# Kernel tuning notes

Hardware: AMD Instinct MI355X
Metric: run time of the kernel (lower is better)

## Reference

```python
import jax, jax.numpy as jnp
import numpy as np

N, F_IN, C, H, L = 4096, 768, 256, 4, 2
DH = C // H  # 64 per-head dim for GATv2


def _ln(x, g, b, eps=1e-5):
    mu = x.mean(-1, keepdims=True)
    var = ((x - mu) ** 2).mean(-1, keepdims=True)
    return (x - mu) / jnp.sqrt(var + eps) * g + b


def _gat_layer(x, wl, wr, att, b, src, dst):
    # GATv2Conv: e_ij = att . leaky_relu(Wl x_j + Wr x_i); softmax over incoming j; concat heads.
    xs = (x @ wl).reshape(N, H, DH)  # source transform
    xd = (x @ wr).reshape(N, H, DH)  # target transform
    e = jnp.einsum('ehd,hd->eh', jax.nn.leaky_relu(xs[src] + xd[dst], 0.2), att)  # [E,H]
    m = jax.ops.segment_max(e, dst, num_segments=N)          # segment softmax (stable)
    p = jnp.exp(e - m[dst])
    s = jax.ops.segment_sum(p, dst, num_segments=N)
    alpha = p / (s[dst] + 1e-16)                             # [E,H]
    out = jax.ops.segment_sum(alpha[:, :, None] * xs[src], dst, num_segments=N)
    return out.reshape(N, C) + b


def _mha(x, wq, wk, wv, bq, bk, bv, wo, bo):
    # nn.MultiheadAttention, batch=1 sequence of all news nodes, eval mode.
    q = (x @ wq + bq).reshape(N, H, DH)
    k = (x @ wk + bk).reshape(N, H, DH)
    v = (x @ wv + bv).reshape(N, H, DH)
    scale = np.float32(1.0 / np.sqrt(DH))
    a = jax.nn.softmax(jnp.einsum('nhd,mhd->hnm', q, k) * scale, axis=-1)  # [H,N,N]
    o = jnp.einsum('hnm,mhd->nhd', a, v).reshape(N, C)
    return o @ wo + bo


def setup_inputs() -> dict:
    key = jax.random.key(0)
    ks = jax.random.split(key, 32)
    rn = lambda k, shp: (jax.random.normal(k, shp, dtype=jnp.float32) * 0.02)
    inp = {
        'x': jax.random.normal(ks[0], (N, F_IN), dtype=jnp.float32),
        'edge_index': jax.random.randint(ks[1], (2, N * 64), 0, N, dtype=jnp.int64),
        'emb_w': rn(ks[2], (F_IN, C)), 'emb_b': jnp.zeros((C,), jnp.float32),
        'g1_wl': rn(ks[3], (C, C)), 'g1_wr': rn(ks[4], (C, C)),
        'g1_att': rn(ks[5], (H, DH)), 'g1_b': jnp.zeros((C,), jnp.float32),
        'g2_wl': rn(ks[6], (C, C)), 'g2_wr': rn(ks[7], (C, C)),
        'g2_att': rn(ks[8], (H, DH)), 'g2_b': jnp.zeros((C,), jnp.float32),
        'mha_wq': rn(ks[9], (C, C)), 'mha_wk': rn(ks[10], (C, C)), 'mha_wv': rn(ks[11], (C, C)),
        'mha_bq': jnp.zeros((C,), jnp.float32), 'mha_bk': jnp.zeros((C,), jnp.float32),
        'mha_bv': jnp.zeros((C,), jnp.float32),
        'mha_wo': rn(ks[12], (C, C)), 'mha_bo': jnp.zeros((C,), jnp.float32),
        'ln_g': jnp.ones((C,), jnp.float32), 'ln_b': jnp.zeros((C,), jnp.float32),
        'cls_w1': rn(ks[13], (C, C // 2)), 'cls_b1': jnp.zeros((C // 2,), jnp.float32),
        'cls_w2': rn(ks[14], (C // 2, 2)), 'cls_b2': jnp.zeros((2,), jnp.float32),
    }
    return inp


def reference(x, edge_index, emb_w, emb_b, g1_wl, g1_wr, g1_att, g1_b,
              g2_wl, g2_wr, g2_att, g2_b, mha_wq, mha_wk, mha_wv, mha_bq,
              mha_bk, mha_bv, mha_wo, mha_bo, ln_g, ln_b,
              cls_w1, cls_b1, cls_w2, cls_b2):
    # add self loops (GATv2Conv default add_self_loops=True)
    loops = jnp.arange(N, dtype=edge_index.dtype)
    src = jnp.concatenate([edge_index[0], loops])
    dst = jnp.concatenate([edge_index[1], loops])

    h = x @ emb_w + emb_b                              # node embedding Linear(-1, C)
    h = jax.nn.relu(_gat_layer(h, g1_wl, g1_wr, g1_att, g1_b, src, dst))
    h = jax.nn.relu(_gat_layer(h, g2_wl, g2_wr, g2_att, g2_b, src, dst))

    # entity-aware self-attention + residual LayerNorm
    enh = _mha(h, mha_wq, mha_wk, mha_wv, mha_bq, mha_bk, mha_bv, mha_wo, mha_bo)
    h = _ln(h + enh, ln_g, ln_b)

    # classifier MLP (dropout = identity in eval)
    h = jax.nn.relu(h @ cls_w1 + cls_b1)
    return h @ cls_w2 + cls_b2
```

## Files before the change

kernel.cpp:

```cpp
#include <hip/hip_runtime.h>

typedef __attribute__((ext_vector_type(8))) short short8_t;
typedef __attribute__((ext_vector_type(4))) float f32x4_t;

#define N_NODES  4096
#define E0_EDGES 262144
#define E_TOTAL  266240
#define SPLITS   8
#define KV_PER_SPLIT (N_NODES / SPLITS)
#define BUCKET_CAP 160

__device__ __forceinline__ float bf2f(unsigned short u){
  union { unsigned int i; float f; } v; v.i = ((unsigned int)u) << 16; return v.f;
}
__device__ __forceinline__ unsigned short f2bf(float f){
  union { float f; unsigned int i; } v; v.f = f;
  unsigned int r = (v.i + 0x7FFFu + ((v.i >> 16) & 1u)) >> 16;
  return (unsigned short)r;
}
__device__ __forceinline__ unsigned int cvtpk_bf16(float lo, float hi){
  unsigned int r;
  asm volatile("v_cvt_pk_bf16_f32 %0, %1, %2" : "=v"(r) : "v"(lo), "v"(hi));
  return r;
}
template<int CTRL>
__device__ __forceinline__ float dpp_add(float x){
  int v = __builtin_amdgcn_update_dpp(0, __float_as_int(x), CTRL, 0xF, 0xF, true);
  return x + __int_as_float(v);
}
__device__ __forceinline__ float rowsum16(float x){
  x = dpp_add<0xB1>(x); x = dpp_add<0x4E>(x); x = dpp_add<0x124>(x); x = dpp_add<0x128>(x);
  return x;
}
__device__ __forceinline__ void wg_barrier(){
  asm volatile("s_waitcnt lgkmcnt(0)" ::: "memory");
  __builtin_amdgcn_s_barrier();
  asm volatile("" ::: "memory");
}
__device__ __forceinline__ uint4 cvt8_f32_to_bf16(float4 f0, float4 f1){
  union { unsigned short u[8]; uint4 q; } o;
  o.u[0]=f2bf(f0.x); o.u[1]=f2bf(f0.y); o.u[2]=f2bf(f0.z); o.u[3]=f2bf(f0.w);
  o.u[4]=f2bf(f1.x); o.u[5]=f2bf(f1.y); o.u[6]=f2bf(f1.z); o.u[7]=f2bf(f1.w);
  return o.q;
}

struct TJob { const float* src; unsigned short* dst; int rows, cols, tile0; };
struct TJobs { TJob j[10]; };

__global__ __launch_bounds__(256) void prep_kernel(const float* __restrict__ x, unsigned short* __restrict__ xb,
                                                   TJobs jobs, int tb, int* __restrict__ zp){
  __shared__ unsigned short tile[64 * 64];
  int b = blockIdx.x, t = threadIdx.x;
  if (b < 3072){
    int i = (b * 256 + t) * 4;
    float4 v = *(const float4*)&x[i];
    union { unsigned short u[4]; uint2 q; } o;
    o.u[0] = f2bf(v.x); o.u[1] = f2bf(v.y); o.u[2] = f2bf(v.z); o.u[3] = f2bf(v.w);
    *(uint2*)&xb[i] = o.q;
    return;
  }
  if (b < 3072 + tb){
    int bb = b - 3072;
    int ji = 0;
    #pragma unroll
    for (int k = 1; k < 10; k++) if (bb >= jobs.j[k].tile0) ji = k;
    TJob J = jobs.j[ji];
    int lt = bb - J.tile0;
    int tpr = J.cols >> 6;
    int tr = lt / tpr, tc = lt - tr * tpr;
    #pragma unroll
    for (int i2 = 0; i2 < 2; i2++){
      int e = i2 * 2048 + t * 8;
      int nl = e >> 6, c8 = e & 63;
      const float* sp = &J.src[(size_t)(tr * 64 + nl) * J.cols + tc * 64 + c8];
      float4 v0 = *(const float4*)sp;
      float4 v1 = *(const float4*)(sp + 4);
      *(uint4*)&tile[nl * 64 + (((c8 >> 3) ^ ((nl >> 3) & 7)) * 8)] = cvt8_f32_to_bf16(v0, v1);
    }
    __syncthreads();
    #pragma unroll
    for (int i2 = 0; i2 < 2; i2++){
      int e = i2 * 2048 + t * 8;
      int cl = e >> 6, n8 = e & 63;
      union { unsigned short u[8]; uint4 q; } o;
      #pragma unroll
      for (int j = 0; j < 8; j++){
        int row = n8 + j;
        o.u[j] = tile[row * 64 + (((cl >> 3) ^ ((row >> 3) & 7)) * 8) + (cl & 7)];
      }
      *(uint4*)&J.dst[(size_t)(tc * 64 + cl) * J.rows + tr * 64 + n8] = o.q;
    }
    return;
  }
  int i = (b - 3072 - tb) * 256 + t;
  if (i < N_NODES) zp[i] = 0;
}

__global__ __launch_bounds__(256) void scatter_kernel(const int* __restrict__ ei, int* __restrict__ cnt,
                                                      int* __restrict__ csrc){
  int e = blockIdx.x * 256 + threadIdx.x;
  if (e >= E_TOTAL) return;
  int s, d;
  if (e < E0_EDGES){ s = ei[e]; d = ei[E0_EDGES + e]; }
  else { s = d = e - E0_EDGES; }
  int pos = atomicAdd(&cnt[d], 1);
  csrc[d * BUCKET_CAP + pos] = s;
}

struct GJob { const unsigned short* Wt; const float* bias; float* outF; unsigned short* outB; unsigned short* outT; float scale; };
struct GJobs { GJob j[3]; };

__global__ __launch_bounds__(256) void gemm_kernel(const unsigned short* __restrict__ A, GJobs jobs,
                                                   int K, int Nc, int relu){
  __shared__ unsigned short lds[8192];
  const int t = threadIdx.x;
  const GJob job = jobs.j[blockIdx.z];
  const int lane = t & 63, w = t >> 6;
  const int wm = w >> 1, wn = w & 1;
  const int c16 = lane & 15, g = lane >> 4;
  const int bm = blockIdx.x, bn = blockIdx.y;

  const int srow = t >> 2, schunk = t & 3;
  const unsigned short* Ag = A      + (size_t)(bm * 64 + srow) * K + schunk * 8;
  const unsigned short* Bg = job.Wt + (size_t)(bn * 64 + srow) * K + schunk * 8;
  const int swz = srow * 32 + ((schunk ^ ((srow >> 1) & 3)) * 8);

  const int arow0 = wm * 32 + c16, arow1 = arow0 + 16;
  const int aoff0 = arow0 * 32 + ((g ^ ((arow0 >> 1) & 3)) * 8);
  const int aoff1 = arow1 * 32 + ((g ^ ((arow1 >> 1) & 3)) * 8);
  const int bcol0 = wn * 32 + c16, bcol1 = bcol0 + 16;
  const int boff0 = 2048 + bcol0 * 32 + ((g ^ ((bcol0 >> 1) & 3)) * 8);
  const int boff1 = 2048 + bcol1 * 32 + ((g ^ ((bcol1 >> 1) & 3)) * 8);

  f32x4_t acc[2][2] = {};
  const int nk = K >> 5;

  {
    uint4 av = *(const uint4*)(Ag);
    uint4 bv = *(const uint4*)(Bg);
    *(uint4*)&lds[swz]        = av;
    *(uint4*)&lds[2048 + swz] = bv;
  }
  int cur = 0;
  for (int i = 0; i < nk; i++){
    const bool pf = (i + 1) < nk;
    uint4 av, bv;
    if (pf){
      av = *(const uint4*)(Ag + (i + 1) * 32);
      bv = *(const uint4*)(Bg + (i + 1) * 32);
    }
    wg_barrier();
    const int base = cur * 4096;
    union { uint4 u; short8_t s; } a0, a1, b0, b1;
    a0.u = *(const uint4*)&lds[base + aoff0];
    a1.u = *(const uint4*)&lds[base + aoff1];
    b0.u = *(const uint4*)&lds[base + boff0];
    b1.u = *(const uint4*)&lds[base + boff1];
    acc[0][0] = __builtin_amdgcn_mfma_f32_16x16x32_bf16(a0.s, b0.s, acc[0][0], 0, 0, 0);
    acc[0][1] = __builtin_amdgcn_mfma_f32_16x16x32_bf16(a0.s, b1.s, acc[0][1], 0, 0, 0);
    acc[1][0] = __builtin_amdgcn_mfma_f32_16x16x32_bf16(a1.s, b0.s, acc[1][0], 0, 0, 0);
    acc[1][1] = __builtin_amdgcn_mfma_f32_16x16x32_bf16(a1.s, b1.s, acc[1][1], 0, 0, 0);
    if (pf){
      const int nb = (cur ^ 1) * 4096;
      *(uint4*)&lds[nb + swz]        = av;
      *(uint4*)&lds[nb + 2048 + swz] = bv;
      cur ^= 1;
    }
  }

  #pragma unroll
  for (int fm = 0; fm < 2; fm++){
    #pragma unroll
    for (int fn = 0; fn < 2; fn++){
      int col = bn * 64 + wn * 32 + fn * 16 + c16;
      float bia = job.bias ? job.bias[col] : 0.f;
      float vv[4];
      #pragma unroll
      for (int r = 0; r < 4; r++){
        float v = (acc[fm][fn][r] + bia) * job.scale;
        if (relu) v = fmaxf(v, 0.f);
        vv[r] = v;
      }
      int row0 = bm * 64 + wm * 32 + fm * 16 + g * 4;
      if (job.outF){
        #pragma unroll
        for (int r = 0; r < 4; r++) job.outF[(size_t)(row0 + r) * Nc + col] = vv[r];
      }
      if (job.outB){
        #pragma unroll
        for (int r = 0; r < 4; r++) job.outB[(size_t)(row0 + r) * Nc + col] = f2bf(vv[r]);
      }
      if (job.outT){
        union { unsigned short u[4]; uint2 q; } pk;
        #pragma unroll
        for (int r = 0; r < 4; r++) pk.u[r] = f2bf(vv[r]);
        *(uint2*)&job.outT[(size_t)col * 4096 + row0] = pk.q;
      }
    }
  }
}

__global__ __launch_bounds__(256) void gat_gather(const unsigned short* __restrict__ xs, const unsigned short* __restrict__ xd,
                                                  const float* __restrict__ att, const float* __restrict__ bias,
                                                  const int* __restrict__ cnt, const int* __restrict__ csrc,
                                                  unsigned short* __restrict__ outB, float* __restrict__ outF){
  __shared__ float combL[4][256];
  __shared__ float combS[4][4];
  const int i = blockIdx.x, t = threadIdx.x;
  const int lane = t & 63, w = t >> 6;
  float xdc[4], attc[4];
  {
    uint2 xv = *(const uint2*)&xd[i * 256 + lane * 4];
    xdc[0] = bf2f((unsigned short)(xv.x & 0xffff)); xdc[1] = bf2f((unsigned short)(xv.x >> 16));
    xdc[2] = bf2f((unsigned short)(xv.y & 0xffff)); xdc[3] = bf2f((unsigned short)(xv.y >> 16));
    float4 av = *(const float4*)&att[lane * 4];
    attc[0] = av.x; attc[1] = av.y; attc[2] = av.z; attc[3] = av.w;
  }
  const int b1 = cnt[i];
  const int* bucket = csrc + i * BUCKET_CAP;
  float acc0 = 0.f, acc1 = 0.f, acc2 = 0.f, acc3 = 0.f, ssum = 0.f;
  int p = w;
  for (; p + 4 < b1; p += 8){
    int sA = bucket[p], sB = bucket[p + 4];
    uint2 xa = *(const uint2*)&xs[sA * 256 + lane * 4];
    uint2 xb = *(const uint2*)&xs[sB * 256 + lane * 4];
    float a0 = bf2f((unsigned short)(xa.x & 0xffff)), a1 = bf2f((unsigned short)(xa.x >> 16));
    float a2 = bf2f((unsigned short)(xa.y & 0xffff)), a3 = bf2f((unsigned short)(xa.y >> 16));
    float b0_ = bf2f((unsigned short)(xb.x & 0xffff)), b1_ = bf2f((unsigned short)(xb.x >> 16));
    float b2_ = bf2f((unsigned short)(xb.y & 0xffff)), b3_ = bf2f((unsigned short)(xb.y >> 16));
    float va0 = a0 + xdc[0]; va0 = (va0 > 0.f) ? va0 : 0.2f * va0;
    float va1 = a1 + xdc[1]; va1 = (va1 > 0.f) ? va1 : 0.2f * va1;
    float va2 = a2 + xdc[2]; va2 = (va2 > 0.f) ? va2 : 0.2f * va2;
    float va3 = a3 + xdc[3]; va3 = (va3 > 0.f) ? va3 : 0.2f * va3;
    float vb0 = b0_ + xdc[0]; vb0 = (vb0 > 0.f) ? vb0 : 0.2f * vb0;
    float vb1 = b1_ + xdc[1]; vb1 = (vb1 > 0.f) ? vb1 : 0.2f * vb1;
    float vb2 = b2_ + xdc[2]; vb2 = (vb2 > 0.f) ? vb2 : 0.2f * vb2;
    float vb3 = b3_ + xdc[3]; vb3 = (vb3 > 0.f) ? vb3 : 0.2f * vb3;
    float eA = rowsum16(va0 * attc[0] + va1 * attc[1] + va2 * attc[2] + va3 * attc[3]);
    float eB = rowsum16(vb0 * attc[0] + vb1 * attc[1] + vb2 * attc[2] + vb3 * attc[3]);
    float pA = __expf(eA), pB = __expf(eB);
    ssum += pA + pB;
    acc0 += pA * a0 + pB * b0_; acc1 += pA * a1 + pB * b1_;
    acc2 += pA * a2 + pB * b2_; acc3 += pA * a3 + pB * b3_;
  }
  if (p < b1){
    int s = bucket[p];
    uint2 xv = *(const uint2*)&xs[s * 256 + lane * 4];
    float x0 = bf2f((unsigned short)(xv.x & 0xffff)), x1 = bf2f((unsigned short)(xv.x >> 16));
    float x2 = bf2f((unsigned short)(xv.y & 0xffff)), x3 = bf2f((unsigned short)(xv.y >> 16));
    float v0 = x0 + xdc[0]; v0 = (v0 > 0.f) ? v0 : 0.2f * v0;
    float v1 = x1 + xdc[1]; v1 = (v1 > 0.f) ? v1 : 0.2f * v1;
    float v2 = x2 + xdc[2]; v2 = (v2 > 0.f) ? v2 : 0.2f * v2;
    float v3 = x3 + xdc[3]; v3 = (v3 > 0.f) ? v3 : 0.2f * v3;
    float e = rowsum16(v0 * attc[0] + v1 * attc[1] + v2 * attc[2] + v3 * attc[3]);
    float pe = __expf(e);
    ssum += pe;
    acc0 += pe * x0; acc1 += pe * x1; acc2 += pe * x2; acc3 += pe * x3;
  }
  combL[w][lane * 4 + 0] = acc0; combL[w][lane * 4 + 1] = acc1;
  combL[w][lane * 4 + 2] = acc2; combL[w][lane * 4 + 3] = acc3;
  if ((lane & 15) == 0) combS[w][lane >> 4] = ssum;
  __syncthreads();
  float atot = combL[0][t] + combL[1][t] + combL[2][t] + combL[3][t];
  int hh = t >> 6;
  float stot = combS[0][hh] + combS[1][hh] + combS[2][hh] + combS[3][hh];
  float o = atot / (stot + 1e-16f) + bias[t];
  o = fmaxf(o, 0.f);
  outB[i * 256 + t] = f2bf(o);
  if (outF) outF[i * 256 + t] = o;
}

__global__ __launch_bounds__(512, 2) void attn_kernel(const unsigned short* __restrict__ qb, const unsigned short* __restrict__ kb,
                                                      const unsigned short* __restrict__ vt,
                                                      _Float16* __restrict__ Opart, float* __restrict__ Ol){
  __shared__ unsigned short K_lds[2][4096];
  __shared__ unsigned short V_lds[2][4096];
  __shared__ unsigned short P_lds[8][2048];
  const int t = threadIdx.x, lane = t & 63, w = t >> 6;
  const int c16 = lane & 15, g = lane >> 4;
  const int h = blockIdx.y, bq = blockIdx.x, sp = blockIdx.z;

  const int sr = t >> 3, sc = (t & 7) * 8;
  const int kw = sr * 64 + (((t & 7) ^ ((sr >> 1) & 7)) * 8);
  const int vw = sr * 64 + (((t & 7) ^ (sr & 7)) * 8);

  short8_t qa[2][2];
  #pragma unroll
  for (int qm = 0; qm < 2; qm++){
    int qrow = bq * 256 + w * 32 + qm * 16 + c16;
    union { uint4 u; short8_t s; } cv0, cv1;
    cv0.u = *(const uint4*)&qb[(size_t)qrow * 256 + h * 64 + g * 8];
    cv1.u = *(const uint4*)&qb[(size_t)qrow * 256 + h * 64 + 32 + g * 8];
    qa[qm][0] = cv0.s; qa[qm][1] = cv1.s;
  }

  f32x4_t oacc[2][4] = {};
  float lsum[2] = {0.f, 0.f};

  const int kv_lo = sp * KV_PER_SPLIT;
  {
    uint4 k0 = *(const uint4*)&kb[(size_t)(kv_lo + sr) * 256 + h * 64 + sc];
    uint4 v0 = *(const uint4*)&vt[(size_t)(h * 64 + sr) * 4096 + kv_lo + sc];
    *(uint4*)&K_lds[0][kw] = k0;
    *(uint4*)&V_lds[0][vw] = v0;
  }
  int cur = 0;

  for (int ti = 0; ti < KV_PER_SPLIT / 64; ti++){
    const bool pf = (ti + 1) < KV_PER_SPLIT / 64;
    uint4 nk, nv;
    if (pf){
      int kvn = kv_lo + (ti + 1) * 64;
      nk = *(const uint4*)&kb[(size_t)(kvn + sr) * 256 + h * 64 + sc];
      nv = *(const uint4*)&vt[(size_t)(h * 64 + sr) * 4096 + kvn + sc];
    }
    wg_barrier();
    const unsigned short* Kb = K_lds[cur];
    const unsigned short* Vb = V_lds[cur];
    unsigned short* Pw = P_lds[w];

    f32x4_t sacc[2][4] = {};
    #pragma unroll
    for (int kd = 0; kd < 2; kd++){
      #pragma unroll
      for (int fn = 0; fn < 4; fn++){
        union { uint4 u; short8_t s; } kf;
        kf.u = *(const uint4*)&Kb[(fn * 16 + c16) * 64 + (((kd * 4 + g) ^ ((c16 >> 1) & 7)) * 8)];
        sacc[0][fn] = __builtin_amdgcn_mfma_f32_16x16x32_bf16(kf.s, qa[0][kd], sacc[0][fn], 0, 0, 0);
        sacc[1][fn] = __builtin_amdgcn_mfma_f32_16x16x32_bf16(kf.s, qa[1][kd], sacc[1][fn], 0, 0, 0);
      }
    }

    #pragma unroll
    for (int qm = 0; qm < 2; qm++){
      float ps = 0.f;
      int row = qm * 16 + c16;
      #pragma unroll
      for (int fn = 0; fn < 4; fn++){
        float p0 = __builtin_exp2f(sacc[qm][fn][0]);
        float p1 = __builtin_exp2f(sacc[qm][fn][1]);
        float p2 = __builtin_exp2f(sacc[qm][fn][2]);
        float p3 = __builtin_exp2f(sacc[qm][fn][3]);
        ps += (p0 + p1) + (p2 + p3);
        uint2 pk;
        pk.x = cvtpk_bf16(p0, p1);
        pk.y = cvtpk_bf16(p2, p3);
        int chunk = (fn * 2 + (g >> 1)) ^ (c16 & 7);
        *(uint2*)&Pw[row * 64 + chunk * 8 + (g & 1) * 4] = pk;
      }
      ps += __shfl_xor(ps, 16, 64);
      ps += __shfl_xor(ps, 32, 64);
      lsum[qm] += ps;
    }

    #pragma unroll
    for (int kd2 = 0; kd2 < 2; kd2++){
      const int ch = (((kd2 * 4 + g) ^ (c16 & 7)) * 8);
      union { uint4 u; short8_t s; } pt0, pt1;
      pt0.u = *(const uint4*)&Pw[c16 * 64 + ch];
      pt1.u = *(const uint4*)&Pw[(16 + c16) * 64 + ch];
      #pragma unroll
      for (int fn = 0; fn < 4; fn++){
        union { uint4 u; short8_t s; } vf;
        vf.u = *(const uint4*)&Vb[(fn * 16 + c16) * 64 + ch];
        oacc[0][fn] = __builtin_amdgcn_mfma_f32_16x16x32_bf16(vf.s, pt0.s, oacc[0][fn], 0, 0, 0);
        oacc[1][fn] = __builtin_amdgcn_mfma_f32_16x16x32_bf16(vf.s, pt1.s, oacc[1][fn], 0, 0, 0);
      }
    }

    if (pf){
      *(uint4*)&K_lds[cur ^ 1][kw] = nk;
      *(uint4*)&V_lds[cur ^ 1][vw] = nv;
      cur ^= 1;
    }
  }

  const int sh = sp * 4 + h;
  #pragma unroll
  for (int qm = 0; qm < 2; qm++){
    int node = bq * 256 + w * 32 + qm * 16 + c16;
    #pragma unroll
    for (int fn = 0; fn < 4; fn++){
      union { _Float16 h[4]; uint2 q; } pk;
      #pragma unroll
      for (int r = 0; r < 4; r++) pk.h[r] = (_Float16)oacc[qm][fn][r];
      *(uint2*)&Opart[((size_t)sh * N_NODES + node) * 64 + fn * 16 + g * 4] = pk.q;
    }
    if (g == 0) Ol[(size_t)sh * N_NODES + node] = lsum[qm];
  }
}

__global__ __launch_bounds__(256) void wo_ln_cls_kernel(const _Float16* __restrict__ Opart, const float* __restrict__ Ol,
                                                        const unsigned short* __restrict__ Wt, const float* __restrict__ bo,
                                                        const float* __restrict__ h2f, const float* __restrict__ gg,
                                                        const float* __restrict__ bb,
                                                        const unsigned short* __restrict__ Wt1, const float* __restrict__ b1,
                                                        const float* __restrict__ w2, const float* __restrict__ b2,
                                                        float* __restrict__ out){
  __shared__ unsigned short Ab[2][512];
  __shared__ unsigned short Bb[2][8192];
  __shared__ unsigned short Cb[2][4096];
  __shared__ unsigned short hl[16 * 264];
  __shared__ float red1[4][16], red2[4][16];
  __shared__ float cred0[4][16], cred1[4][16];
  __shared__ float Ls[64];
  const int t = threadIdx.x, lane = t & 63, w = t >> 6;
  const int c16 = lane & 15, g = lane >> 4;
  const int bm = blockIdx.x;

  const int arow = t >> 2, achk = t & 3;
  const int aswz = arow * 32 + ((achk ^ ((arow >> 1) & 3)) * 8);
  const int bq_ = t >> 2, bchk = t & 3;

  if (t < 64){
    int node = bm * 16 + (t >> 2), h = t & 3;
    float L = 0.f;
    #pragma unroll
    for (int s = 0; s < SPLITS; s++) L += Ol[(size_t)(s * 4 + h) * N_NODES + node];
    Ls[t] = 1.f / L;
  }
  __syncthreads();

  const int afr = c16 * 32 + ((g ^ ((c16 >> 1) & 3)) * 8);
  int bfr[4];
  #pragma unroll
  for (int fn = 0; fn < 4; fn++){
    int col = w * 64 + fn * 16 + c16;
    bfr[fn] = col * 32 + ((g ^ ((col >> 1) & 3)) * 8);
  }

  const int anode = bm * 16 + arow;
  auto loadA = [&](int k0, uint4* pa){
    int c0 = k0 + achk * 8;
    int hh = c0 >> 6, d0 = c0 & 63;
    #pragma unroll
    for (int s = 0; s < SPLITS; s++)
      pa[s] = *(const uint4*)&Opart[((size_t)(s * 4 + hh) * N_NODES + anode) * 64 + d0];
  };
  auto packA = [&](int k0, const uint4* pa) -> uint4 {
    float a[8] = {0.f,0.f,0.f,0.f,0.f,0.f,0.f,0.f};
    #pragma unroll
    for (int s = 0; s < SPLITS; s++){
      union { uint4 q; _Float16 h[8]; } u; u.q = pa[s];
      #pragma unroll
      for (int j = 0; j < 8; j++) a[j] += (float)u.h[j];
    }
    int c0 = k0 + achk * 8;
    float Li = Ls[(arow << 2) | (c0 >> 6)];
    union { unsigned short u[8]; uint4 q; } o;
    #pragma unroll
    for (int j = 0; j < 8; j++) o.u[j] = f2bf(a[j] * Li);
    return o.q;
  };

  f32x4_t acc[4] = {};
  {
    if (t < 64){
      uint4 pa0[SPLITS];
      loadA(0, pa0);
      *(uint4*)&Ab[0][aswz] = packA(0, pa0);
    }
    #pragma unroll
    for (int j = 0; j < 4; j++){
      int col = j * 64 + bq_;
      *(uint4*)&Bb[0][col * 32 + ((bchk ^ ((col >> 1) & 3)) * 8)] = *(const uint4*)&Wt[(size_t)col * 256 + bchk * 8];
    }
  }
  int cur = 0;
  for (int i = 0; i < 8; i++){
    const bool pf = i < 7;
    uint4 pa[SPLITS]; uint4 pb[4];
    int k1 = (i + 1) * 32;
    if (pf){
      if (t < 64) loadA(k1, pa);
      #pragma unroll
      for (int j = 0; j < 4; j++){
        int col = j * 64 + bq_;
        pb[j] = *(const uint4*)&Wt[(size_t)col * 256 + k1 + bchk * 8];
      }
    }
    wg_barrier();
    union { uint4 u; short8_t s; } a, b;
    a.u = *(const uint4*)&Ab[cur][afr];
    #pragma unroll
    for (int fn = 0; fn < 4; fn++){
      b.u = *(const uint4*)&Bb[cur][bfr[fn]];
      acc[fn] = __builtin_amdgcn_mfma_f32_16x16x32_bf16(a.s, b.s, acc[fn], 0, 0, 0);
    }
    if (pf){
      if (t < 64) *(uint4*)&Ab[cur ^ 1][aswz] = packA(k1, pa);
      #pragma unroll
      for (int j = 0; j < 4; j++){
        int col = j * 64 + bq_;
        *(uint4*)&Bb[cur ^ 1][col * 32 + ((bchk ^ ((col >> 1) & 3)) * 8)] = pb[j];
      }
      cur ^= 1;
    }
  }

  float vv[4][4];
  #pragma unroll
  for (int fn = 0; fn < 4; fn++){
    int col = w * 64 + fn * 16 + c16;
    float bia = bo[col];
    #pragma unroll
    for (int r = 0; r < 4; r++)
      vv[fn][r] = acc[fn][r] + bia + h2f[(size_t)(bm * 16 + g * 4 + r) * 256 + col];
  }
  #pragma unroll
  for (int r = 0; r < 4; r++){
    float a = 0.f, b = 0.f;
    #pragma unroll
    for (int fn = 0; fn < 4; fn++){ a += vv[fn][r]; b += vv[fn][r] * vv[fn][r]; }
    a = rowsum16(a); b = rowsum16(b);
    if (c16 == 0){ red1[w][g * 4 + r] = a; red2[w][g * 4 + r] = b; }
  }
  __syncthreads();
  #pragma unroll
  for (int r = 0; r < 4; r++){
    int row = g * 4 + r;
    float S1 = red1[0][row] + red1[1][row] + red1[2][row] + red1[3][row];
    float S2 = red2[0][row] + red2[1][row] + red2[2][row] + red2[3][row];
    float mean = S1 * (1.f / 256.f);
    float var = S2 * (1.f / 256.f) - mean * mean;
    float rs = rsqrtf(var + 1e-5f);
    #pragma unroll
    for (int fn = 0; fn < 4; fn++){
      int col = w * 64 + fn * 16 + c16;
      hl[row * 264 + col] = f2bf((vv[fn][r] - mean) * rs * gg[col] + bb[col]);
    }
  }

  wg_barrier();
  int cfr[2];
  #pragma unroll
  for (int fn = 0; fn < 2; fn++){
    int col = w * 32 + fn * 16 + c16;
    cfr[fn] = col * 32 + ((g ^ ((col >> 1) & 3)) * 8);
  }
  f32x4_t cacc[2] = {};
  {
    #pragma unroll
    for (int j = 0; j < 2; j++){
      int col = j * 64 + bq_;
      *(uint4*)&Cb[0][col * 32 + ((bchk ^ ((col >> 1) & 3)) * 8)] = *(const uint4*)&Wt1[(size_t)col * 256 + bchk * 8];
    }
  }
  cur = 0;
  for (int i = 0; i < 8; i++){
    const bool pf = i < 7;
    uint4 pb[2];
    if (pf){
      int k1 = (i + 1) * 32;
      #pragma unroll
      for (int j = 0; j < 2; j++){
        int col = j * 64 + bq_;
        pb[j] = *(const uint4*)&Wt1[(size_t)col * 256 + k1 + bchk * 8];
      }
    }
    wg_barrier();
    union { uint4 u; short8_t s; } a, b;
    a.u = *(const uint4*)&hl[c16 * 264 + i * 32 + g * 8];
    #pragma unroll
    for (int fn = 0; fn < 2; fn++){
      b.u = *(const uint4*)&Cb[cur][cfr[fn]];
      cacc[fn] = __builtin_amdgcn_mfma_f32_16x16x32_bf16(a.s, b.s, cacc[fn], 0, 0, 0);
    }
    if (pf){
      #pragma unroll
      for (int j = 0; j < 2; j++){
        int col = j * 64 + bq_;
        *(uint4*)&Cb[cur ^ 1][col * 32 + ((bchk ^ ((col >> 1) & 3)) * 8)] = pb[j];
      }
      cur ^= 1;
    }
  }
  float cv[2][4];
  #pragma unroll
  for (int fn = 0; fn < 2; fn++){
    int col = w * 32 + fn * 16 + c16;
    float bia = b1[col];
    #pragma unroll
    for (int r = 0; r < 4; r++) cv[fn][r] = fmaxf(cacc[fn][r] + bia, 0.f);
  }
  float w20 = w2[(w * 32 + c16) * 2],      w21 = w2[(w * 32 + c16) * 2 + 1];
  float w30 = w2[(w * 32 + 16 + c16) * 2], w31 = w2[(w * 32 + 16 + c16) * 2 + 1];
  #pragma unroll
  for (int r = 0; r < 4; r++){
    float a0 = cv[0][r] * w20 + cv[1][r] * w30;
    float a1 = cv[0][r] * w21 + cv[1][r] * w31;
    a0 = rowsum16(a0); a1 = rowsum16(a1);
    if (c16 == 0){ cred0[w][g * 4 + r] = a0; cred1[w][g * 4 + r] = a1; }
  }
  __syncthreads();
  if (t < 16){
    float q0 = cred0[0][t] + cred0[1][t] + cred0[2][t] + cred0[3][t] + b2[0];
    float q1 = cred1[0][t] + cred1[1][t] + cred1[2][t] + cred1[3][t] + b2[1];
    out[(size_t)(bm * 16 + t) * 2]     = q0;
    out[(size_t)(bm * 16 + t) * 2 + 1] = q1;
  }
}

extern "C" void kernel_launch(void* const* d_in, const int* in_sizes, int n_in,
                              void* d_out, int out_size, void* d_ws, size_t ws_size,
                              hipStream_t stream){
  const float* x      = (const float*)d_in[0];
  const int*   ei     = (const int*)d_in[1];
  const float* emb_w  = (const float*)d_in[2];
  const float* emb_b  = (const float*)d_in[3];
  const float* g1_wl  = (const float*)d_in[4];
  const float* g1_wr  = (const float*)d_in[5];
  const float* g1_att = (const float*)d_in[6];
  const float* g1_b   = (const float*)d_in[7];
  const float* g2_wl  = (const float*)d_in[8];
  const float* g2_wr  = (const float*)d_in[9];
  const float* g2_att = (const float*)d_in[10];
  const float* g2_b   = (const float*)d_in[11];
  const float* wq     = (const float*)d_in[12];
  const float* wk     = (const float*)d_in[13];
  const float* wv     = (const float*)d_in[14];
  const float* bq     = (const float*)d_in[15];
  const float* bk     = (const float*)d_in[16];
  const float* bv     = (const float*)d_in[17];
  const float* wo     = (const float*)d_in[18];
  const float* bo     = (const float*)d_in[19];
  const float* ln_g   = (const float*)d_in[20];
  const float* ln_b   = (const float*)d_in[21];
  const float* cls_w1 = (const float*)d_in[22];
  const float* cls_b1 = (const float*)d_in[23];
  const float* cls_w2 = (const float*)d_in[24];
  const float* cls_b2 = (const float*)d_in[25];
  float* out = (float*)d_out;

  char* wsb = (char*)d_ws;
  size_t o = 0;
  auto take = [&](size_t bytes) -> char* {
    char* r = wsb + o; o += (bytes + 255) & ~(size_t)255; return r;
  };
  unsigned short* wt_emb  = (unsigned short*)take(768 * 256 * 2);
  unsigned short* wt_wl1  = (unsigned short*)take(256 * 256 * 2);
  unsigned short* wt_wr1  = (unsigned short*)take(256 * 256 * 2);
  unsigned short* wt_wl2  = (unsigned short*)take(256 * 256 * 2);
  unsigned short* wt_wr2  = (unsigned short*)take(256 * 256 * 2);
  unsigned short* wt_wq   = (unsigned short*)take(256 * 256 * 2);
  unsigned short* wt_wk   = (unsigned short*)take(256 * 256 * 2);
  unsigned short* wt_wv   = (unsigned short*)take(256 * 256 * 2);
  unsigned short* wt_wo   = (unsigned short*)take(256 * 256 * 2);
  unsigned short* wt_cls1 = (unsigned short*)take(256 * 128 * 2);
  unsigned short* x_bf    = (unsigned short*)take((size_t)4096 * 768 * 2);
  unsigned short* h0_bf   = (unsigned short*)take((size_t)4096 * 256 * 2);
  unsigned short* xs1_bf  = (unsigned short*)take((size_t)4096 * 256 * 2);
  unsigned short* xd1_bf  = (unsigned short*)take((size_t)4096 * 256 * 2);
  unsigned short* h1_bf   = (unsigned short*)take((size_t)4096 * 256 * 2);
  unsigned short* xs2_bf  = (unsigned short*)take((size_t)4096 * 256 * 2);
  unsigned short* xd2_bf  = (unsigned short*)take((size_t)4096 * 256 * 2);
  unsigned short* h2_bf   = (unsigned short*)take((size_t)4096 * 256 * 2);
  float*          h2_f    = (float*)take((size_t)4096 * 256 * 4);
  unsigned short* q_bf    = (unsigned short*)take((size_t)4096 * 256 * 2);
  unsigned short* k_bf    = (unsigned short*)take((size_t)4096 * 256 * 2);
  unsigned short* vt_bf   = (unsigned short*)take((size_t)4096 * 256 * 2);
  int* cnt  = (int*)take(4096 * 4);
  int* csrc = (int*)take((size_t)N_NODES * BUCKET_CAP * 4);
  _Float16* Opart = (_Float16*)take((size_t)SPLITS * 4 * N_NODES * 64 * 2);
  float*    Ol    = (float*)take((size_t)SPLITS * 4 * N_NODES * 4);

  TJobs TJ;
  TJob tj[10] = {
    { emb_w,  wt_emb,  768, 256, 0 },
    { g1_wl,  wt_wl1,  256, 256, 0 },
    { g1_wr,  wt_wr1,  256, 256, 0 },
    { g2_wl,  wt_wl2,  256, 256, 0 },
    { g2_wr,  wt_wr2,  256, 256, 0 },
    { wq,     wt_wq,   256, 256, 0 },
    { wk,     wt_wk,   256, 256, 0 },
    { wv,     wt_wv,   256, 256, 0 },
    { wo,     wt_wo,   256, 256, 0 },
    { cls_w1, wt_cls1, 256, 128, 0 },
  };
  int tb = 0;
  for (int i = 0; i < 10; i++){
    tj[i].tile0 = tb;
    tb += (tj[i].rows >> 6) * (tj[i].cols >> 6);
    TJ.j[i] = tj[i];
  }
  prep_kernel<<<3072 + tb + 16, 256, 0, stream>>>(x, x_bf, TJ, tb, cnt);

  scatter_kernel<<<(E_TOTAL + 255) / 256, 256, 0, stream>>>(ei, cnt, csrc);

  GJobs J;
  J = {}; J.j[0] = { wt_emb, emb_b, nullptr, h0_bf, nullptr, 1.f };
  gemm_kernel<<<dim3(64, 4, 1), 256, 0, stream>>>(x_bf, J, 768, 256, 0);
  J = {}; J.j[0] = { wt_wl1, nullptr, nullptr, xs1_bf, nullptr, 1.f }; J.j[1] = { wt_wr1, nullptr, nullptr, xd1_bf, nullptr, 1.f };
  gemm_kernel<<<dim3(64, 4, 2), 256, 0, stream>>>(h0_bf, J, 256, 256, 0);
  gat_gather<<<4096, 256, 0, stream>>>(xs1_bf, xd1_bf, g1_att, g1_b, cnt, csrc, h1_bf, nullptr);
  J = {}; J.j[0] = { wt_wl2, nullptr, nullptr, xs2_bf, nullptr, 1.f }; J.j[1] = { wt_wr2, nullptr, nullptr, xd2_bf, nullptr, 1.f };
  gemm_kernel<<<dim3(64, 4, 2), 256, 0, stream>>>(h1_bf, J, 256, 256, 0);
  gat_gather<<<4096, 256, 0, stream>>>(xs2_bf, xd2_bf, g2_att, g2_b, cnt, csrc, h2_bf, h2_f);
  J = {};
  J.j[0] = { wt_wq, bq, nullptr, q_bf, nullptr, 0.125f * 1.44269504f };
  J.j[1] = { wt_wk, bk, nullptr, k_bf, nullptr, 1.f };
  J.j[2] = { wt_wv, bv, nullptr, nullptr, vt_bf, 1.f };
  gemm_kernel<<<dim3(64, 4, 3), 256, 0, stream>>>(h2_bf, J, 256, 256, 0);
  attn_kernel<<<dim3(16, 4, SPLITS), 512, 0, stream>>>(q_bf, k_bf, vt_bf, Opart, Ol);
  wo_ln_cls_kernel<<<256, 256, 0, stream>>>(Opart, Ol, wt_wo, bo, h2_f, ln_g, ln_b,
                                            wt_cls1, cls_b1, cls_w2, cls_b2, out);

  (void)in_sizes; (void)n_in; (void)out_size; (void)ws_size;
}
```

Baseline: 153.5 us.

## Double attention KV splits, remap blocks for XCD locality, stream split combine

Raises the number of KV splits in the attention kernel from 8 to 16 to launch more blocks and fill the CUs better. It switches to a 1D grid whose index remap places blocks sharing the same head and split on the same XCD, for better L2 reuse of K and V. It also raises the launch-bounds minimum to 8 blocks. The output-projection kernel now sums the partial results as it loads them, so it no longer holds all partials in registers. The trade-off is that the combine stage reads twice as many fp16 partials. The higher launch-bounds minimum may also squeeze the register budget, which could cause spills.

```diff
diff --git a/kernel.cpp b/kernel.cpp
--- a/kernel.cpp
+++ b/kernel.cpp
@@ -6,7 +6,7 @@
 #define N_NODES  4096
 #define E0_EDGES 262144
 #define E_TOTAL  266240
-#define SPLITS   8
+#define SPLITS   16
 #define KV_PER_SPLIT (N_NODES / SPLITS)
 #define BUCKET_CAP 160
 
@@ -270,7 +270,7 @@
   if (outF) outF[i * 256 + t] = o;
 }
 
-__global__ __launch_bounds__(512, 2) void attn_kernel(const unsigned short* __restrict__ qb, const unsigned short* __restrict__ kb,
+__global__ __launch_bounds__(512, 8) void attn_kernel(const unsigned short* __restrict__ qb, const unsigned short* __restrict__ kb,
                                                       const unsigned short* __restrict__ vt,
                                                       _Float16* __restrict__ Opart, float* __restrict__ Ol){
   __shared__ unsigned short K_lds[2][4096];
@@ -278,7 +278,10 @@
   __shared__ unsigned short P_lds[8][2048];
   const int t = threadIdx.x, lane = t & 63, w = t >> 6;
   const int c16 = lane & 15, g = lane >> 4;
-  const int h = blockIdx.y, bq = blockIdx.x, sp = blockIdx.z;
+  const int L = blockIdx.x;
+  const int g64 = (L & 7) * 8 + (L >> 7);
+  const int bq = (L >> 3) & 15;
+  const int h = g64 & 3, sp = g64 >> 2;
 
   const int sr = t >> 3, sc = (t & 7) * 8;
   const int kw = sr * 64 + (((t & 7) ^ ((sr >> 1) & 7)) * 8);
@@ -430,23 +433,18 @@
   }
 
   const int anode = bm * 16 + arow;
-  auto loadA = [&](int k0, uint4* pa){
+  auto combineA = [&](int k0) -> uint4 {
     int c0 = k0 + achk * 8;
     int hh = c0 >> 6, d0 = c0 & 63;
-    #pragma unroll
-    for (int s = 0; s < SPLITS; s++)
-      pa[s] = *(const uint4*)&Opart[((size_t)(s * 4 + hh) * N_NODES + anode) * 64 + d0];
-  };
-  auto packA = [&](int k0, const uint4* pa) -> uint4 {
     float a[8] = {0.f,0.f,0.f,0.f,0.f,0.f,0.f,0.f};
     #pragma unroll
     for (int s = 0; s < SPLITS; s++){
-      union { uint4 q; _Float16 h[8]; } u; u.q = pa[s];
+      union { uint4 q; _Float16 h[8]; } u;
+      u.q = *(const uint4*)&Opart[((size_t)(s * 4 + hh) * N_NODES + anode) * 64 + d0];
       #pragma unroll
       for (int j = 0; j < 8; j++) a[j] += (float)u.h[j];
     }
-    int c0 = k0 + achk * 8;
-    float Li = Ls[(arow << 2) | (c0 >> 6)];
+    float Li = Ls[(arow << 2) | hh];
     union { unsigned short u[8]; uint4 q; } o;
     #pragma unroll
     for (int j = 0; j < 8; j++) o.u[j] = f2bf(a[j] * Li);
@@ -455,11 +453,7 @@
 
   f32x4_t acc[4] = {};
   {
-    if (t < 64){
-      uint4 pa0[SPLITS];
-      loadA(0, pa0);
-      *(uint4*)&Ab[0][aswz] = packA(0, pa0);
-    }
+    if (t < 64) *(uint4*)&Ab[0][aswz] = combineA(0);
     #pragma unroll
     for (int j = 0; j < 4; j++){
       int col = j * 64 + bq_;
@@ -469,10 +463,11 @@
   int cur = 0;
   for (int i = 0; i < 8; i++){
     const bool pf = i < 7;
-    uint4 pa[SPLITS]; uint4 pb[4];
+    uint4 pb[4];
+    uint4 av;
     int k1 = (i + 1) * 32;
     if (pf){
-      if (t < 64) loadA(k1, pa);
+      if (t < 64) av = combineA(k1);
       #pragma unroll
       for (int j = 0; j < 4; j++){
         int col = j * 64 + bq_;
@@ -488,7 +483,7 @@
       acc[fn] = __builtin_amdgcn_mfma_f32_16x16x32_bf16(a.s, b.s, acc[fn], 0, 0, 0);
     }
     if (pf){
-      if (t < 64) *(uint4*)&Ab[cur ^ 1][aswz] = packA(k1, pa);
+      if (t < 64) *(uint4*)&Ab[cur ^ 1][aswz] = av;
       #pragma unroll
       for (int j = 0; j < 4; j++){
         int col = j * 64 + bq_;
@@ -701,7 +696,7 @@
   J.j[1] = { wt_wk, bk, nullptr, k_bf, nullptr, 1.f };
   J.j[2] = { wt_wv, bv, nullptr, nullptr, vt_bf, 1.f };
   gemm_kernel<<<dim3(64, 4, 3), 256, 0, stream>>>(h2_bf, J, 256, 256, 0);
-  attn_kernel<<<dim3(16, 4, SPLITS), 512, 0, stream>>>(q_bf, k_bf, vt_bf, Opart, Ol);
+  attn_kernel<<<16 * 4 * SPLITS, 512, 0, stream>>>(q_bf, k_bf, vt_bf, Opart, Ol);
   wo_ln_cls_kernel<<<256, 256, 0, stream>>>(Opart, Ol, wt_wo, bo, h2_f, ln_g, ln_b,
                                             wt_cls1, cls_b1, cls_w2, cls_b2, out);
 
```

Measured after the change: 173.5 us. +13.0%, slower.
